# Performance work log

Measured on AMD Instinct MI355X. Metric: run time of the kernel, lower is better.

## Reference

```python
import jax, jax.numpy as jnp
import numpy as np

QMAX = 7.0            # int4 narrow range: [-7, 7]
SCALING_MIN_VAL = 2e-16


def fake_quant_weight_per_channel(w):
    """Brevitas CommonIntWeightPerChannelQuant, bit_width=4.

    Per-output-channel float scale from abs-max stats, narrow-range signed
    int4 round+clamp, then dequantize. STE so gradients pass through.
    w: [O, I, KH, KW]
    """
    amax = jnp.max(jnp.abs(w), axis=(1, 2, 3), keepdims=True)   # [O,1,1,1]
    scale = jnp.maximum(amax / QMAX, SCALING_MIN_VAL)
    wq = jnp.clip(jnp.round(w / scale), -QMAX, QMAX) * scale
    # straight-through estimator (matches Brevitas round_ste backward)
    return w + jax.lax.stop_gradient(wq - w)


def setup_inputs() -> dict:
    key = jax.random.key(0)
    kx, kw = jax.random.split(key)
    x = jax.random.normal(kx, (32, 256, 56, 56), dtype=jnp.float32)
    # conv weight [out_channels, in_channels, kh, kw]
    w = jax.random.normal(kw, (256, 256, 3, 3), dtype=jnp.float32) * 0.05
    return {"x": x, "w": w}


def reference(x, w):
    wq = fake_quant_weight_per_channel(w)
    return jax.lax.conv_general_dilated(
        x, wq,
        window_strides=(1, 1),
        padding=((1, 1), (1, 1)),
        dimension_numbers=("NCHW", "OIHW", "NCHW"),
    )
```

## Files before the change

kernel.cpp:

```cpp
#include <hip/hip_runtime.h>
#include <cstdint>
#include <cstddef>

typedef __bf16 bf16x8 __attribute__((ext_vector_type(8)));
typedef float  f32x4  __attribute__((ext_vector_type(4)));
typedef float  f32x16 __attribute__((ext_vector_type(16)));
typedef int    i32x4  __attribute__((ext_vector_type(4)));

#define QMAX 7.0f
#define SCALE_MIN 2e-16f

#define BAR()     asm volatile("s_barrier" ::: "memory")
#define WAITVM(N) asm volatile("s_waitcnt vmcnt(" #N ")" ::: "memory")

__global__ __launch_bounds__(256) void quant_w_kernel(const float* __restrict__ w,
                                                      __bf16* __restrict__ wq) {
    const int o = blockIdx.x;
    const int t = threadIdx.x;
    const float* wo = w + (size_t)o * 2304;

    float vals[9];
    float m = 0.f;
    #pragma unroll
    for (int i = 0; i < 9; ++i) {
        float v = wo[t + i * 256];
        vals[i] = v;
        m = fmaxf(m, fabsf(v));
    }
    #pragma unroll
    for (int off = 32; off >= 1; off >>= 1) m = fmaxf(m, __shfl_down(m, off));
    __shared__ float red[4];
    __shared__ float s_scale;
    if ((t & 63) == 0) red[t >> 6] = m;
    __syncthreads();
    if (t == 0) {
        float am = fmaxf(fmaxf(red[0], red[1]), fmaxf(red[2], red[3]));
        s_scale = fmaxf(am / QMAX, SCALE_MIN);
    }
    __syncthreads();
    const float scale = s_scale;

    #pragma unroll
    for (int i = 0; i < 9; ++i) {
        int idx = t + i * 256;
        int c = idx / 9;
        int tap = idx - c * 9;
        float q = rintf(vals[i] / scale);
        q = fminf(QMAX, fmaxf(-QMAX, q));
        wq[(size_t)tap * 65536 + (size_t)o * 256 + c] = (__bf16)(q * scale);
    }
}

__global__ __launch_bounds__(256) void convert_x_kernel(const float* __restrict__ x,
                                                        __bf16* __restrict__ xpad) {
    __shared__ float tile[32][33];
    const int n  = blockIdx.z;
    const int c0 = blockIdx.y * 32;
    const int p0 = blockIdx.x * 32;
    const int tx = threadIdx.x & 31;
    const int ty = threadIdx.x >> 5;

    #pragma unroll
    for (int r = 0; r < 4; ++r) {
        int c = c0 + ty + r * 8;
        tile[ty + r * 8][tx] = x[((size_t)(n * 256 + c)) * 3136 + p0 + tx];
    }
    __syncthreads();
    #pragma unroll
    for (int r = 0; r < 4; ++r) {
        int p = p0 + ty + r * 8;
        int h = p / 56, wcol = p - h * 56;
        xpad[(((size_t)n * 58 + h + 1) * 58 + (wcol + 1)) * 256 + c0 + tx] =
            (__bf16)tile[tx][ty + r * 8];
    }
}

__global__ __launch_bounds__(256) void zero_halo_kernel(__bf16* __restrict__ xpad) {
    const int t = blockIdx.x * 256 + threadIdx.x;
    const int cvec = t & 31;
    const int r    = t >> 5;
    const int n    = r / 228;
    const int pos  = r - n * 228;
    if (n >= 32) return;
    int h, wcol;
    if      (pos < 58)  { h = 0;          wcol = pos; }
    else if (pos < 116) { h = 57;         wcol = pos - 58; }
    else if (pos < 172) { h = pos - 115;  wcol = 0; }
    else                { h = pos - 171;  wcol = 57; }
    i32x4* dst = (i32x4*)(xpad + (((size_t)n * 58 + h) * 58 + wcol) * 256);
    dst[cvec] = (i32x4){0, 0, 0, 0};
}

__device__ __forceinline__ void gload_lds16(const void* g, void* l) {
    __builtin_amdgcn_global_load_lds((const __attribute__((address_space(1))) void*)g,
                                     (__attribute__((address_space(3))) void*)l,
                                     16, 0, 0);
}

__global__ __launch_bounds__(256, 2) void conv_mfma_kernel(const __bf16* __restrict__ xpad,
                                                           const __bf16* __restrict__ wq,
                                                           float* __restrict__ out) {
    extern __shared__ __align__(16) char lds[];
    const int tid  = threadIdx.x;
    const int wv   = tid >> 6;
    const int lane = tid & 63;
    const int bid  = blockIdx.x;
    const int swz  = (bid & 7) * 196 + (bid >> 3);
    const int ptile = swz >> 1;
    const int ohalf = swz & 1;
    const int p0   = ptile * 128;
    const int o0   = ohalf * 128;

    const int wm = wv >> 1;
    const int wn = wv & 1;

    const int schunk = (lane & 7) ^ (lane >> 3);
    const __bf16* pAg = wq + (size_t)(o0 + wv * 8 + (lane >> 3)) * 256 + schunk * 8;
    const __bf16* pB[4];
    #pragma unroll
    for (int j = 0; j < 4; ++j) {
        int row = (wv & 1) * 64 + (j >> 1) * 32 + (j & 1) * 16 + (wv >> 1) * 8 + (lane >> 3);
        int pos = p0 + row;
        int ni = pos / 3136;
        int hw = pos - ni * 3136;
        int h = hw / 56, w = hw - h * 56;
        pB[j] = xpad + (((size_t)ni * 58 + h) * 58 + w) * 256 + schunk * 8;
    }
    const int adst = wv * 1024;
    const int bdst = 16384 + (wv & 1) * 8192 + (wv >> 1) * 1024;

    const int hi = lane >> 5;
    int kxo[4];
    #pragma unroll
    for (int ks = 0; ks < 4; ++ks)
        kxo[ks] = ((ks * 2 + hi) ^ (lane & 7)) * 16;
    const int arowb = (wm * 64 + (lane & 31)) * 128;
    const int browb = 16384 + (wn * 64 + (lane & 31)) * 128;

    f32x16 acc[2][2];
    #pragma unroll
    for (int m = 0; m < 2; ++m)
        #pragma unroll
        for (int n = 0; n < 2; ++n)
            acc[m][n] = (f32x16)(0.f);

    {
        char* buf = lds;
        gload_lds16(pAg + 0 * 8192, buf + adst + 0 * 4096);
        gload_lds16(pAg + 1 * 8192, buf + adst + 1 * 4096);
        gload_lds16(pAg + 2 * 8192, buf + adst + 2 * 4096);
        gload_lds16(pAg + 3 * 8192, buf + adst + 3 * 4096);
        gload_lds16(pB[0],          buf + bdst + 0 * 4096 + 0 * 2048);
        gload_lds16(pB[1],          buf + bdst + 0 * 4096 + 1 * 2048);
        gload_lds16(pB[2],          buf + bdst + 1 * 4096 + 0 * 2048);
        gload_lds16(pB[3],          buf + bdst + 1 * 4096 + 1 * 2048);
    }

    for (int s = 0; s < 36; ++s) {
        const char* Rd = lds + ((s & 1) ? 32768 : 0);
        char*       Wr = lds + ((s & 1) ? 0 : 32768);
        const bool stg = (s < 35);
        size_t aoffN = 0, boffN = 0;
        if (stg) {
            const int sn = s + 1;
            const int tapN = sn >> 2, ccN = sn & 3;
            const int khN = tapN / 3, kwN = tapN - khN * 3;
            aoffN = (size_t)tapN * 65536 + ccN * 64;
            boffN = (size_t)(khN * 58 + kwN) * 256 + ccN * 64;
        }

        bf16x8 a0[4], a1[4], b[4];

        WAITVM(2);
        BAR();
        #pragma unroll
        for (int ks = 0; ks < 4; ++ks) {
            a0[ks] = *(const bf16x8*)(Rd + arowb + 0 * 4096 + kxo[ks]);
            a1[ks] = *(const bf16x8*)(Rd + arowb + 1 * 4096 + kxo[ks]);
            b[ks]  = *(const bf16x8*)(Rd + browb + 0 * 4096 + kxo[ks]);
        }
        if (stg) {
            gload_lds16(pAg + 0 * 8192 + aoffN, Wr + adst + 0 * 4096);
            gload_lds16(pAg + 1 * 8192 + aoffN, Wr + adst + 1 * 4096);
            gload_lds16(pAg + 2 * 8192 + aoffN, Wr + adst + 2 * 4096);
            gload_lds16(pAg + 3 * 8192 + aoffN, Wr + adst + 3 * 4096);
            gload_lds16(pB[0] + boffN,          Wr + bdst + 0 * 2048);
            gload_lds16(pB[1] + boffN,          Wr + bdst + 2048);
        }
        __builtin_amdgcn_s_setprio(1);
        #pragma unroll
        for (int ks = 0; ks < 4; ++ks) {
            acc[0][0] = __builtin_amdgcn_mfma_f32_32x32x16_bf16(a0[ks], b[ks], acc[0][0], 0, 0, 0);
            acc[1][0] = __builtin_amdgcn_mfma_f32_32x32x16_bf16(a1[ks], b[ks], acc[1][0], 0, 0, 0);
        }
        __builtin_amdgcn_s_setprio(0);

        if (stg) { WAITVM(6); } else { WAITVM(0); }
        BAR();
        #pragma unroll
        for (int ks = 0; ks < 4; ++ks)
            b[ks] = *(const bf16x8*)(Rd + browb + 1 * 4096 + kxo[ks]);
        if (stg) {
            gload_lds16(pB[2] + boffN, Wr + bdst + 4096);
            gload_lds16(pB[3] + boffN, Wr + bdst + 4096 + 2048);
        }
        __builtin_amdgcn_s_setprio(1);
        #pragma unroll
        for (int ks = 0; ks < 4; ++ks) {
            acc[0][1] = __builtin_amdgcn_mfma_f32_32x32x16_bf16(a0[ks], b[ks], acc[0][1], 0, 0, 0);
            acc[1][1] = __builtin_amdgcn_mfma_f32_32x32x16_bf16(a1[ks], b[ks], acc[1][1], 0, 0, 0);
        }
        __builtin_amdgcn_s_setprio(0);
        BAR();
    }

    #pragma unroll
    for (int n = 0; n < 2; ++n) {
        const int pos = p0 + wn * 64 + n * 32 + (lane & 31);
        const int ni = pos / 3136;
        const int hw = pos - ni * 3136;
        float* ob = out + (size_t)ni * 802816 + hw;
        #pragma unroll
        for (int m = 0; m < 2; ++m) {
            const int om = o0 + wm * 64 + m * 32 + 4 * hi;
            #pragma unroll
            for (int r = 0; r < 16; ++r) {
                const int o = om + (r & 3) + 8 * (r >> 2);
                ob[(size_t)o * 3136] = acc[m][n][r];
            }
        }
    }
}

__global__ __launch_bounds__(256) void conv_naive_kernel(const float* __restrict__ x,
                                                         const float* __restrict__ w,
                                                         float* __restrict__ out) {
    const int n = blockIdx.z;
    const int o = blockIdx.y;
    const int strip = blockIdx.x;
    __shared__ float wqs[2304];
    __shared__ float red[4];
    __shared__ float s_scale;
    const float* wo = w + (size_t)o * 2304;
    float m = 0.f;
    for (int i = threadIdx.x; i < 2304; i += 256) m = fmaxf(m, fabsf(wo[i]));
    #pragma unroll
    for (int off = 32; off >= 1; off >>= 1) m = fmaxf(m, __shfl_down(m, off));
    if ((threadIdx.x & 63) == 0) red[threadIdx.x >> 6] = m;
    __syncthreads();
    if (threadIdx.x == 0) {
        float am = fmaxf(fmaxf(red[0], red[1]), fmaxf(red[2], red[3]));
        s_scale = fmaxf(am / QMAX, SCALE_MIN);
    }
    __syncthreads();
    const float scale = s_scale;
    for (int i = threadIdx.x; i < 2304; i += 256) {
        float q = rintf(wo[i] / scale);
        q = fminf(QMAX, fmaxf(-QMAX, q));
        wqs[i] = q * scale;
    }
    __syncthreads();
    int p = strip * 256 + threadIdx.x;
    if (p >= 3136) return;
    int h = p / 56, wcol = p - h * 56;
    float acc = 0.f;
    for (int c = 0; c < 256; ++c) {
        const float* xc = x + ((size_t)(n * 256 + c)) * 3136;
        const float* wk = wqs + c * 9;
        #pragma unroll
        for (int kh = 0; kh < 3; ++kh) {
            int hh = h + kh - 1;
            if (hh < 0 || hh > 55) continue;
            #pragma unroll
            for (int kw = 0; kw < 3; ++kw) {
                int ww2 = wcol + kw - 1;
                if (ww2 < 0 || ww2 > 55) continue;
                acc += xc[hh * 56 + ww2] * wk[kh * 3 + kw];
            }
        }
    }
    out[((size_t)(n * 256 + o)) * 3136 + p] = acc;
}

extern "C" void kernel_launch(void* const* d_in, const int* in_sizes, int n_in,
                              void* d_out, int out_size, void* d_ws, size_t ws_size,
                              hipStream_t stream) {
    const float* x = (const float*)d_in[0];
    const float* w = (const float*)d_in[1];
    float* out = (float*)d_out;

    const size_t WQ_BYTES   = 9ull * 256 * 256 * 2;
    const size_t XPAD_OFF   = WQ_BYTES;
    const size_t XPAD_BYTES = 32ull * 58 * 58 * 256 * 2;

    if (ws_size >= XPAD_OFF + XPAD_BYTES) {
        __bf16* wq   = (__bf16*)d_ws;
        __bf16* xpad = (__bf16*)((char*)d_ws + XPAD_OFF);
        hipFuncSetAttribute((const void*)conv_mfma_kernel,
                            hipFuncAttributeMaxDynamicSharedMemorySize, 65536);
        zero_halo_kernel<<<912, 256, 0, stream>>>(xpad);
        quant_w_kernel<<<256, 256, 0, stream>>>(w, wq);
        convert_x_kernel<<<dim3(98, 8, 32), 256, 0, stream>>>(x, xpad);
        conv_mfma_kernel<<<1568, 256, 65536, stream>>>(xpad, wq, out);
    } else {
        conv_naive_kernel<<<dim3(13, 256, 32), 256, 0, stream>>>(x, w, out);
    }
}
```

Baseline: 174.8 us.

## Use a triple-buffered K=32 pipeline with smaller LDS stages for higher occupancy

The convolution GEMM main loop now uses 72 K-steps of 32 channels instead of 36 steps of 64. Each step is 16KB of LDS, arranged as a three-slot ring buffer totalling 48KB instead of two 32KB buffers. Each step issues the next stage's loads before waiting and needs one barrier instead of three. The LDS swizzle and row layouts change to match, and launch bounds rise to 3 blocks per CU so more waves can hide latency. The cost is twice as many loop iterations, each doing fewer MFMAs per barrier, and a tighter register budget.

```diff
diff --git a/kernel.cpp b/kernel.cpp
--- a/kernel.cpp
+++ b/kernel.cpp
@@ -97,7 +97,7 @@
                                      16, 0, 0);
 }
 
-__global__ __launch_bounds__(256, 2) void conv_mfma_kernel(const __bf16* __restrict__ xpad,
+__global__ __launch_bounds__(256, 3) void conv_mfma_kernel(const __bf16* __restrict__ xpad,
                                                            const __bf16* __restrict__ wq,
                                                            float* __restrict__ out) {
     extern __shared__ __align__(16) char lds[];
@@ -114,28 +114,36 @@
     const int wm = wv >> 1;
     const int wn = wv & 1;
 
-    const int schunk = (lane & 7) ^ (lane >> 3);
-    const __bf16* pAg = wq + (size_t)(o0 + wv * 8 + (lane >> 3)) * 256 + schunk * 8;
-    const __bf16* pB[4];
-    #pragma unroll
-    for (int j = 0; j < 4; ++j) {
-        int row = (wv & 1) * 64 + (j >> 1) * 32 + (j & 1) * 16 + (wv >> 1) * 8 + (lane >> 3);
-        int pos = p0 + row;
+    const int trow   = tid >> 2;
+    const int schunk = (tid & 3) ^ ((tid >> 5) & 3);
+    const __bf16* pA[2];
+    #pragma unroll
+    for (int j = 0; j < 2; ++j)
+        pA[j] = wq + (size_t)(o0 + j * 64 + trow) * 256 + schunk * 8;
+    const __bf16* pBs[2];
+    #pragma unroll
+    for (int j = 0; j < 2; ++j) {
+        int pos = p0 + j * 64 + trow;
         int ni = pos / 3136;
         int hw = pos - ni * 3136;
         int h = hw / 56, w = hw - h * 56;
-        pB[j] = xpad + (((size_t)ni * 58 + h) * 58 + w) * 256 + schunk * 8;
+        pBs[j] = xpad + (((size_t)ni * 58 + h) * 58 + w) * 256 + schunk * 8;
     }
     const int adst = wv * 1024;
-    const int bdst = 16384 + (wv & 1) * 8192 + (wv >> 1) * 1024;
-
-    const int hi = lane >> 5;
-    int kxo[4];
-    #pragma unroll
-    for (int ks = 0; ks < 4; ++ks)
-        kxo[ks] = ((ks * 2 + hi) ^ (lane & 7)) * 16;
-    const int arowb = (wm * 64 + (lane & 31)) * 128;
-    const int browb = 16384 + (wn * 64 + (lane & 31)) * 128;
+    const int bdst = 8192 + wv * 1024;
+
+    const int l31 = lane & 31;
+    const int lk  = lane >> 5;
+    const int rsw = (lane >> 3) & 3;
+    int kx[2];
+    #pragma unroll
+    for (int ks = 0; ks < 2; ++ks)
+        kx[ks] = ((ks * 2 + lk) ^ rsw) * 16;
+    int arow[2], brow[2];
+    #pragma unroll
+    for (int m = 0; m < 2; ++m) arow[m] = (wm * 64 + m * 32 + l31) * 64;
+    #pragma unroll
+    for (int n = 0; n < 2; ++n) brow[n] = 8192 + (wn * 64 + n * 32 + l31) * 64;
 
     f32x16 acc[2][2];
     #pragma unroll
@@ -144,79 +152,79 @@
         for (int n = 0; n < 2; ++n)
             acc[m][n] = (f32x16)(0.f);
 
+    auto stage = [&](int step, char* buf) {
+        const int tap = step >> 3, cc = step & 7;
+        const int kh = tap / 3, kw = tap - kh * 3;
+        const size_t aoff = (size_t)tap * 65536 + cc * 32;
+        const size_t boff = (size_t)(kh * 58 + kw) * 256 + cc * 32;
+        gload_lds16(pA[0]  + aoff, buf + adst);
+        gload_lds16(pA[1]  + aoff, buf + adst + 4096);
+        gload_lds16(pBs[0] + boff, buf + bdst);
+        gload_lds16(pBs[1] + boff, buf + bdst + 4096);
+    };
+
+    stage(0, lds);
+
+    int co = 0;
+    #pragma unroll 1
+    for (int s = 0; s < 71; ++s) {
+        int no = co + 16384; if (no == 49152) no = 0;
+        stage(s + 1, lds + no);
+        WAITVM(4);
+        BAR();
+        const char* B = lds + co;
+        bf16x8 af[2][2], bf[2][2];
+        #pragma unroll
+        for (int m = 0; m < 2; ++m)
+            #pragma unroll
+            for (int ks = 0; ks < 2; ++ks)
+                af[m][ks] = *(const bf16x8*)(B + arow[m] + kx[ks]);
+        #pragma unroll
+        for (int n = 0; n < 2; ++n)
+            #pragma unroll
+            for (int ks = 0; ks < 2; ++ks)
+                bf[n][ks] = *(const bf16x8*)(B + brow[n] + kx[ks]);
+        __builtin_amdgcn_s_setprio(1);
+        #pragma unroll
+        for (int ks = 0; ks < 2; ++ks)
+            #pragma unroll
+            for (int m = 0; m < 2; ++m)
+                #pragma unroll
+                for (int n = 0; n < 2; ++n)
+                    acc[m][n] = __builtin_amdgcn_mfma_f32_32x32x16_bf16(
+                        af[m][ks], bf[n][ks], acc[m][n], 0, 0, 0);
+        __builtin_amdgcn_s_setprio(0);
+        co = no;
+    }
     {
-        char* buf = lds;
-        gload_lds16(pAg + 0 * 8192, buf + adst + 0 * 4096);
-        gload_lds16(pAg + 1 * 8192, buf + adst + 1 * 4096);
-        gload_lds16(pAg + 2 * 8192, buf + adst + 2 * 4096);
-        gload_lds16(pAg + 3 * 8192, buf + adst + 3 * 4096);
-        gload_lds16(pB[0],          buf + bdst + 0 * 4096 + 0 * 2048);
-        gload_lds16(pB[1],          buf + bdst + 0 * 4096 + 1 * 2048);
-        gload_lds16(pB[2],          buf + bdst + 1 * 4096 + 0 * 2048);
-        gload_lds16(pB[3],          buf + bdst + 1 * 4096 + 1 * 2048);
-    }
-
-    for (int s = 0; s < 36; ++s) {
-        const char* Rd = lds + ((s & 1) ? 32768 : 0);
-        char*       Wr = lds + ((s & 1) ? 0 : 32768);
-        const bool stg = (s < 35);
-        size_t aoffN = 0, boffN = 0;
-        if (stg) {
-            const int sn = s + 1;
-            const int tapN = sn >> 2, ccN = sn & 3;
-            const int khN = tapN / 3, kwN = tapN - khN * 3;
-            aoffN = (size_t)tapN * 65536 + ccN * 64;
-            boffN = (size_t)(khN * 58 + kwN) * 256 + ccN * 64;
-        }
-
-        bf16x8 a0[4], a1[4], b[4];
-
-        WAITVM(2);
+        WAITVM(0);
         BAR();
-        #pragma unroll
-        for (int ks = 0; ks < 4; ++ks) {
-            a0[ks] = *(const bf16x8*)(Rd + arowb + 0 * 4096 + kxo[ks]);
-            a1[ks] = *(const bf16x8*)(Rd + arowb + 1 * 4096 + kxo[ks]);
-            b[ks]  = *(const bf16x8*)(Rd + browb + 0 * 4096 + kxo[ks]);
-        }
-        if (stg) {
-            gload_lds16(pAg + 0 * 8192 + aoffN, Wr + adst + 0 * 4096);
-            gload_lds16(pAg + 1 * 8192 + aoffN, Wr + adst + 1 * 4096);
-            gload_lds16(pAg + 2 * 8192 + aoffN, Wr + adst + 2 * 4096);
-            gload_lds16(pAg + 3 * 8192 + aoffN, Wr + adst + 3 * 4096);
-            gload_lds16(pB[0] + boffN,          Wr + bdst + 0 * 2048);
-            gload_lds16(pB[1] + boffN,          Wr + bdst + 2048);
-        }
-        __builtin_amdgcn_s_setprio(1);
-        #pragma unroll
-        for (int ks = 0; ks < 4; ++ks) {
-            acc[0][0] = __builtin_amdgcn_mfma_f32_32x32x16_bf16(a0[ks], b[ks], acc[0][0], 0, 0, 0);
-            acc[1][0] = __builtin_amdgcn_mfma_f32_32x32x16_bf16(a1[ks], b[ks], acc[1][0], 0, 0, 0);
-        }
-        __builtin_amdgcn_s_setprio(0);
-
-        if (stg) { WAITVM(6); } else { WAITVM(0); }
-        BAR();
-        #pragma unroll
-        for (int ks = 0; ks < 4; ++ks)
-            b[ks] = *(const bf16x8*)(Rd + browb + 1 * 4096 + kxo[ks]);
-        if (stg) {
-            gload_lds16(pB[2] + boffN, Wr + bdst + 4096);
-            gload_lds16(pB[3] + boffN, Wr + bdst + 4096 + 2048);
-        }
-        __builtin_amdgcn_s_setprio(1);
-        #pragma unroll
-        for (int ks = 0; ks < 4; ++ks) {
-            acc[0][1] = __builtin_amdgcn_mfma_f32_32x32x16_bf16(a0[ks], b[ks], acc[0][1], 0, 0, 0);
-            acc[1][1] = __builtin_amdgcn_mfma_f32_32x32x16_bf16(a1[ks], b[ks], acc[1][1], 0, 0, 0);
-        }
-        __builtin_amdgcn_s_setprio(0);
-        BAR();
-    }
-
+        const char* B = lds + co;
+        bf16x8 af[2][2], bf[2][2];
+        #pragma unroll
+        for (int m = 0; m < 2; ++m)
+            #pragma unroll
+            for (int ks = 0; ks < 2; ++ks)
+                af[m][ks] = *(const bf16x8*)(B + arow[m] + kx[ks]);
+        #pragma unroll
+        for (int n = 0; n < 2; ++n)
+            #pragma unroll
+            for (int ks = 0; ks < 2; ++ks)
+                bf[n][ks] = *(const bf16x8*)(B + brow[n] + kx[ks]);
+        #pragma unroll
+        for (int ks = 0; ks < 2; ++ks)
+            #pragma unroll
+            for (int m = 0; m < 2; ++m)
+                #pragma unroll
+                for (int n = 0; n < 2; ++n)
+                    acc[m][n] = __builtin_amdgcn_mfma_f32_32x32x16_bf16(
+                        af[m][ks], bf[n][ks], acc[m][n], 0, 0, 0);
+    }
+
+    const int hi = lane >> 5;
     #pragma unroll
     for (int n = 0; n < 2; ++n) {
-        const int pos = p0 + wn * 64 + n * 32 + (lane & 31);
+        const int pos = p0 + wn * 64 + n * 32 + l31;
         const int ni = pos / 3136;
         const int hw = pos - ni * 3136;
         float* ob = out + (size_t)ni * 802816 + hw;
@@ -297,11 +305,11 @@
         __bf16* wq   = (__bf16*)d_ws;
         __bf16* xpad = (__bf16*)((char*)d_ws + XPAD_OFF);
         hipFuncSetAttribute((const void*)conv_mfma_kernel,
-                            hipFuncAttributeMaxDynamicSharedMemorySize, 65536);
+                            hipFuncAttributeMaxDynamicSharedMemorySize, 49152);
         zero_halo_kernel<<<912, 256, 0, stream>>>(xpad);
         quant_w_kernel<<<256, 256, 0, stream>>>(w, wq);
         convert_x_kernel<<<dim3(98, 8, 32), 256, 0, stream>>>(x, xpad);
-        conv_mfma_kernel<<<1568, 256, 65536, stream>>>(xpad, wq, out);
+        conv_mfma_kernel<<<1568, 256, 49152, stream>>>(xpad, wq, out);
     } else {
         conv_naive_kernel<<<dim3(13, 256, 32), 256, 0, stream>>>(x, w, out);
     }
```

New measurement: 184.9 us. 1.06x slower.
